# Optimization experiments

Hardware: AMD Instinct MI355X
Metric: run time of the kernel (lower is better)

Reference implementation:

```python
import jax, jax.numpy as jnp
import numpy as np

L = 5  # number of attention+MLP stages

def _layernorm(x, g, b, eps=1e-5):
    mu = x.mean(-1, keepdims=True)
    var = ((x - mu) ** 2).mean(-1, keepdims=True)
    return (x - mu) * jax.lax.rsqrt(var + eps) * g + b

def setup_inputs() -> dict:
    key = jax.random.key(0)
    B, N, C = 8, 2048, 512  # win_size=4, num_slices=12 -> C = 4*4*384//12 = 512
    ks = jax.random.split(key, 7)
    s = 0.02
    return {
        "x": jax.random.normal(ks[0], (B, N, C), dtype=jnp.float32),
        "qkv_w": jax.random.normal(ks[1], (L, C, 3 * C), dtype=jnp.float32) * s,
        "qkv_b": jnp.zeros((L, 3 * C), dtype=jnp.float32),
        "ln_g": jnp.ones((L, C), dtype=jnp.float32),
        "ln_b": jnp.zeros((L, C), dtype=jnp.float32),
        "fc1_w": jax.random.normal(ks[2], (L, C, 2 * C), dtype=jnp.float32) * s,
        "fc1_b": jnp.zeros((L, 2 * C), dtype=jnp.float32),
        "fc2_w": jax.random.normal(ks[3], (L, 2 * C, C), dtype=jnp.float32) * s,
        "fc2_b": jnp.zeros((L, C), dtype=jnp.float32),
    }

def reference(x, qkv_w, qkv_b, ln_g, ln_b, fc1_w, fc1_b, fc2_w, fc2_b):
    B, N, C = x.shape
    half = N // 2
    scale = C ** -0.5  # num_heads = 1 -> head_dim = C
    # Custom block mask: top-left (half x half) block fully visible,
    # top-right block masked; bottom half is tril with diagonal = N//2,
    # i.e. global row i >= half may attend to columns j <= i.
    i = jnp.arange(N)[:, None]
    j = jnp.arange(N)[None, :]
    allowed = jnp.where(i < half, j < half, j <= i)
    bias = jnp.where(allowed, 0.0, -1000.0).astype(x.dtype)  # (N, N)
    for l in range(L):
        # Mask3dAttention (single head)
        qkv = x @ qkv_w[l] + qkv_b[l]                      # (B, N, 3C)
        q, k, v = jnp.split(qkv, 3, axis=-1)               # each (B, N, C)
        attn = jnp.einsum("bnc,bmc->bnm", q * scale, k) + bias
        attn = jax.nn.softmax(attn, axis=-1)
        x = jnp.einsum("bnm,bmc->bnc", attn, v)
        # residual MLP on normed features
        y = _layernorm(x, ln_g[l], ln_b[l])
        h = jax.nn.gelu(y @ fc1_w[l] + fc1_b[l], approximate=False)
        x = x + (h @ fc2_w[l] + fc2_b[l])
    return x
```

## Files before the change

kernel.cpp:

```cpp
#include <hip/hip_runtime.h>
#include <math.h>

typedef unsigned short u16;
typedef __attribute__((ext_vector_type(8))) short bf16x8;
typedef __attribute__((ext_vector_type(4))) float f32x4;
typedef __attribute__((ext_vector_type(4))) unsigned short u16x4;

#define NLAYERS 5
#define BATCH 8
#define SEQ 2048
#define CH 512
#define ROWS_TOTAL (BATCH * SEQ)
#define HALF (SEQ / 2)
#define ATTN_SCALE 0.04419417382415922f

#define SMEM_U16 32768

__device__ __forceinline__ u16 f2bf(float f) {
    unsigned u = __float_as_uint(f);
    u += 0x7fffu + ((u >> 16) & 1u);
    return (u16)(u >> 16);
}

__device__ __forceinline__ u16x4 pack4(f32x4 v) {
    u16x4 o;
    o.x = f2bf(v[0]); o.y = f2bf(v[1]); o.z = f2bf(v[2]); o.w = f2bf(v[3]);
    return o;
}

__device__ __forceinline__ void st16(u16* p, u16x4 v) { *(u16x4*)p = v; }
__device__ __forceinline__ void st16f(float* p, f32x4 v) { *(f32x4*)p = v; }

__device__ __forceinline__ void llds16(const u16* g, u16* l) {
    __builtin_amdgcn_global_load_lds(
        (const __attribute__((address_space(1))) unsigned int*)g,
        (__attribute__((address_space(3))) unsigned int*)l, 16, 0, 0);
}

__device__ __forceinline__ void xcd_rc(int& rt, int& ct) {
    const int n = blockIdx.x;
    const int m = n >> 3;
    rt = (n & 7) * 16 + (m & 15);
    ct = m >> 4;
}

__device__ __forceinline__ void mm_issue(const u16* gA, const u16* gB,
                                         u16* lA, u16* lB, int lda, int ldb)
{
#pragma unroll
    for (int i = 0; i < 4; ++i)
        llds16(gA + (size_t)i * 32 * lda, lA + i * 2048);
#pragma unroll
    for (int i = 0; i < 4; ++i)
        llds16(gB + (size_t)i * 32 * ldb, lB + i * 2048);
}

__device__ __forceinline__ void mm_compute(const u16* As, const u16* Bs,
                                           const int aoff[2][4],
                                           const int boff[2][4],
                                           f32x4 acc[4][4])
{
#pragma unroll
    for (int h = 0; h < 2; ++h) {
        bf16x8 af[4], bfv[4];
#pragma unroll
        for (int t = 0; t < 4; ++t) af[t]  = *(const bf16x8*)&As[aoff[h][t]];
#pragma unroll
        for (int t = 0; t < 4; ++t) bfv[t] = *(const bf16x8*)&Bs[boff[h][t]];
#pragma unroll
        for (int ti = 0; ti < 4; ++ti)
#pragma unroll
            for (int tj = 0; tj < 4; ++tj)
                acc[ti][tj] = __builtin_amdgcn_mfma_f32_16x16x32_bf16(
                    af[ti], bfv[tj], acc[ti][tj], 0, 0, 0);
    }
}

__device__ __forceinline__ void mm_core(
    const u16* __restrict__ A, int lda,
    const u16* __restrict__ Bt, int ldb,
    int row0, int col0, int K,
    u16* SM, f32x4 acc[4][4])
{
    const int tid  = threadIdx.x;
    const int wave = tid >> 6, lane = tid & 63;
    const int wm = (wave & 1) * 64, wn = (wave >> 1) * 64;
    const int q  = lane >> 4,  ln = lane & 15;

    const int sr8 = lane >> 3;
    const int sc  = (lane & 7) ^ sr8;
    const u16* gA = A  + (size_t)(row0 + wave * 8 + sr8) * lda + sc * 8;
    const u16* gB = Bt + (size_t)(col0 + wave * 8 + sr8) * ldb + sc * 8;

    u16* const A0 = SM;
    u16* const B0 = SM + 8192;
    u16* const A1 = SM + 16384;
    u16* const B1 = SM + 24576;
    u16* const w0a = A0 + wave * 512;
    u16* const w0b = B0 + wave * 512;
    u16* const w1a = A1 + wave * 512;
    u16* const w1b = B1 + wave * 512;

    int aoff[2][4], boff[2][4];
#pragma unroll
    for (int h = 0; h < 2; ++h) {
        const int pos = (((h * 4 + q) ^ (ln & 7)) * 8);
#pragma unroll
        for (int t = 0; t < 4; ++t) {
            aoff[h][t] = (wm + t * 16 + ln) * 64 + pos;
            boff[h][t] = (wn + t * 16 + ln) * 64 + pos;
        }
    }

#pragma unroll
    for (int ti = 0; ti < 4; ++ti)
#pragma unroll
        for (int tj = 0; tj < 4; ++tj)
#pragma unroll
            for (int e = 0; e < 4; ++e) acc[ti][tj][e] = 0.f;

    mm_issue(gA, gB, w0a, w0b, lda, ldb);
    gA += 64; gB += 64;

    for (int k0 = 0; k0 < K; k0 += 128) {
        if (k0 + 64 < K) {
            mm_issue(gA, gB, w1a, w1b, lda, ldb);
            gA += 64; gB += 64;
            asm volatile("s_waitcnt vmcnt(8)" ::: "memory");
        } else {
            asm volatile("s_waitcnt vmcnt(0)" ::: "memory");
        }
        __builtin_amdgcn_s_barrier();
        mm_compute(A0, B0, aoff, boff, acc);
        __builtin_amdgcn_s_barrier();
        __builtin_amdgcn_sched_barrier(0);
        if (k0 + 128 < K) {
            mm_issue(gA, gB, w0a, w0b, lda, ldb);
            gA += 64; gB += 64;
            asm volatile("s_waitcnt vmcnt(8)" ::: "memory");
        } else {
            asm volatile("s_waitcnt vmcnt(0)" ::: "memory");
        }
        __builtin_amdgcn_s_barrier();
        mm_compute(A1, B1, aoff, boff, acc);
        __builtin_amdgcn_s_barrier();
        __builtin_amdgcn_sched_barrier(0);
    }
}

template <typename F>
__device__ __forceinline__ void epi_emit(f32x4 acc[4][4], float* eb, F emit)
{
    const int tid = threadIdx.x, wave = tid >> 6, lane = tid & 63;
    const int wn = (wave >> 1) * 64;
    const int q = lane >> 4, ln = lane & 15;
#pragma unroll
    for (int p = 0; p < 4; ++p) {
        __syncthreads();
        if ((wave & 1) == (p >> 1)) {
            const int tibase = (p & 1) * 2;
#pragma unroll
            for (int tj = 0; tj < 4; ++tj)
#pragma unroll
                for (int t2 = 0; t2 < 2; ++t2)
#pragma unroll
                    for (int r = 0; r < 4; ++r)
                        eb[(t2 * 16 + q * 4 + r) * 132 + wn + tj * 16 + ln] =
                            acc[tibase + t2][tj][r];
        }
        __syncthreads();
#pragma unroll
        for (int s = 0; s < 4; ++s) {
            const int row = s * 8 + (tid >> 5);
            const int col = (tid & 31) * 4;
            f32x4 v = *(const f32x4*)&eb[row * 132 + col];
            emit(p * 32 + row, col, v);
        }
    }
}

__global__ __launch_bounds__(256) void qkv_gemm(
    const u16* __restrict__ A, const u16* __restrict__ Bt,
    const float* __restrict__ bias,
    u16* __restrict__ Qb, u16* __restrict__ Kb, u16* __restrict__ Vt)
{
    __shared__ __align__(16) u16 SMEM[SMEM_U16];
    f32x4 acc[4][4];
    int rt, ct; xcd_rc(rt, ct);
    const int row0 = rt * 128, col0 = ct * 128;
    mm_core(A, CH, Bt, CH, row0, col0, CH, SMEM, acc);

    if (ct < 8) {
        u16* dst = (ct < 4) ? Qb : Kb;
        const int cbase = (ct < 4) ? col0 : col0 - CH;
        const float sc = (ct < 4) ? ATTN_SCALE : 1.0f;
        epi_emit(acc, (float*)SMEM, [&](int row, int col, f32x4 v) {
            const float4 bb = *(const float4*)&bias[col0 + col];
            v[0] = (v[0] + bb.x) * sc; v[1] = (v[1] + bb.y) * sc;
            v[2] = (v[2] + bb.z) * sc; v[3] = (v[3] + bb.w) * sc;
            st16(&dst[(size_t)(row0 + row) * CH + cbase + col], pack4(v));
        });
    } else {
        const int tid = threadIdx.x, wave = tid >> 6, lane = tid & 63;
        const int wm = (wave & 1) * 64, wn = (wave >> 1) * 64;
        const int q = lane >> 4, ln = lane & 15;
#pragma unroll
        for (int tj = 0; tj < 4; ++tj) {
            const int gcol = col0 + wn + tj * 16 + ln;
            const float bv = bias[gcol];
#pragma unroll
            for (int ti = 0; ti < 4; ++ti) {
                const int grow = row0 + wm + ti * 16 + q * 4;
                const int b = grow >> 11, j = grow & (SEQ - 1);
                u16x4 o;
                o.x = f2bf(acc[ti][tj][0] + bv);
                o.y = f2bf(acc[ti][tj][1] + bv);
                o.z = f2bf(acc[ti][tj][2] + bv);
                o.w = f2bf(acc[ti][tj][3] + bv);
                st16(&Vt[(size_t)b * CH * SEQ +
                         (size_t)(gcol - 2 * CH) * SEQ + j], o);
            }
        }
    }
}

__global__ __launch_bounds__(256) void qk_gemm(
    const u16* __restrict__ Qb, const u16* __restrict__ Kb,
    u16* __restrict__ Sb, float* __restrict__ rowsum)
{
    const int id = blockIdx.x;
    const int b = id & 7, jt = (id >> 3) & 15, it = id >> 7;
    if (it < 8) { if (jt >= 8) return; } else if (jt > it) return;
    __shared__ __align__(16) u16 SMEM[SMEM_U16];
    f32x4 acc[4][4];
    const u16* A  = Qb + (size_t)b * SEQ * CH;
    const u16* Bt = Kb + (size_t)b * SEQ * CH;
    u16* S = Sb + (size_t)b * SEQ * SEQ;
    const int row0 = it * 128, col0 = jt * 128;
    mm_core(A, CH, Bt, CH, row0, col0, CH, SMEM, acc);

    const bool upper = (it < 8);
    const int tid = threadIdx.x;
    epi_emit(acc, (float*)SMEM, [&](int row, int col, f32x4 v) {
        const int grow = row0 + row;
        const int gcol = col0 + col;
        f32x4 pv;
#pragma unroll
        for (int e = 0; e < 4; ++e) {
            const bool allowed = upper || (gcol + e <= grow);
            pv[e] = allowed ? __expf(fminf(v[e], 60.f)) : 0.f;
        }
        st16(&S[(size_t)grow * SEQ + gcol], pack4(pv));
        float rs = pv[0] + pv[1] + pv[2] + pv[3];
        rs += __shfl_xor(rs, 1, 64);
        rs += __shfl_xor(rs, 2, 64);
        rs += __shfl_xor(rs, 4, 64);
        rs += __shfl_xor(rs, 8, 64);
        rs += __shfl_xor(rs, 16, 64);
        if ((tid & 31) == 0)
            atomicAdd(&rowsum[b * SEQ + grow], rs);
    });
}

__global__ __launch_bounds__(256) void pv_gemm(
    const u16* __restrict__ Sb, const u16* __restrict__ Vt,
    const float* __restrict__ rowsum, float* __restrict__ O)
{
    const int n = blockIdx.x;
    const int b = n & 7, m = n >> 3;
    const int it = 15 - (m >> 2), ct = m & 3;
    const int Kfull = ((it < 8) ? 8 : (it + 1)) * 128;
    __shared__ __align__(16) u16 SMEM[SMEM_U16];
    f32x4 acc[4][4];
    const u16* A  = Sb + (size_t)b * SEQ * SEQ;
    const u16* Bt = Vt + (size_t)b * CH * SEQ;
    const int row0 = it * 128, col0 = ct * 128;
    mm_core(A, SEQ, Bt, SEQ, row0, col0, Kfull, SMEM, acc);

    epi_emit(acc, (float*)SMEM, [&](int row, int col, f32x4 v) {
        const int grow = row0 + row;
        const float rden = 1.0f / rowsum[b * SEQ + grow];
        v[0] *= rden; v[1] *= rden; v[2] *= rden; v[3] *= rden;
        st16f(&O[(size_t)(b * SEQ + grow) * CH + col0 + col], v);
    });
}

__global__ __launch_bounds__(256) void fc1_gemm(
    const u16* __restrict__ A, const u16* __restrict__ Bt,
    const float* __restrict__ bias, u16* __restrict__ H)
{
    __shared__ __align__(16) u16 SMEM[SMEM_U16];
    f32x4 acc[4][4];
    int rt, ct; xcd_rc(rt, ct);
    const int row0 = rt * 128, col0 = ct * 128;
    mm_core(A, CH, Bt, CH, row0, col0, CH, SMEM, acc);
    epi_emit(acc, (float*)SMEM, [&](int row, int col, f32x4 v) {
        const float4 bb = *(const float4*)&bias[col0 + col];
        v[0] += bb.x; v[1] += bb.y; v[2] += bb.z; v[3] += bb.w;
#pragma unroll
        for (int e = 0; e < 4; ++e)
            v[e] = 0.5f * v[e] * (1.f + erff(v[e] * 0.70710678118654752f));
        st16(&H[(size_t)(row0 + row) * (2 * CH) + col0 + col], pack4(v));
    });
}

template <bool WRITE_X>
__global__ __launch_bounds__(256) void fc2_gemm(
    const u16* __restrict__ A, const u16* __restrict__ Bt,
    const float* __restrict__ bias, float* __restrict__ X,
    u16* __restrict__ Xb)
{
    __shared__ __align__(16) u16 SMEM[SMEM_U16];
    f32x4 acc[4][4];
    int rt, ct; xcd_rc(rt, ct);
    const int row0 = rt * 128, col0 = ct * 128;
    mm_core(A, 2 * CH, Bt, 2 * CH, row0, col0, 2 * CH, SMEM, acc);
    epi_emit(acc, (float*)SMEM, [&](int row, int col, f32x4 v) {
        const size_t idx = (size_t)(row0 + row) * CH + col0 + col;
        const float4 bb = *(const float4*)&bias[col0 + col];
        const f32x4 xv = *(const f32x4*)&X[idx];
        v[0] += bb.x + xv[0]; v[1] += bb.y + xv[1];
        v[2] += bb.z + xv[2]; v[3] += bb.w + xv[3];
        if (WRITE_X) st16f(&X[idx], v);
        st16(&Xb[idx], pack4(v));
    });
}

__device__ __forceinline__ float block_sum(float v, volatile float* red, int tid)
{
#pragma unroll
    for (int off = 1; off < 64; off <<= 1) v += __shfl_xor(v, off, 64);
    __syncthreads();
    if ((tid & 63) == 0) red[tid >> 6] = v;
    __syncthreads();
    return red[0] + red[1] + red[2] + red[3];
}

__global__ __launch_bounds__(256) void ln_kernel(
    const float* __restrict__ x, const float* __restrict__ g,
    const float* __restrict__ bta, u16* __restrict__ y)
{
    __shared__ float red[4];
    const int tid = threadIdx.x;
    const size_t base = (size_t)blockIdx.x * CH;
    float x0 = x[base + tid];
    float x1 = x[base + 256 + tid];
    float mu = block_sum(x0 + x1, red, tid) * (1.f / CH);
    float d0 = x0 - mu, d1 = x1 - mu;
    float var = block_sum(d0 * d0 + d1 * d1, red, tid) * (1.f / CH);
    float w = 1.f / sqrtf(var + 1e-5f);
    y[base + tid]       = f2bf(d0 * w * g[tid]       + bta[tid]);
    y[base + 256 + tid] = f2bf(d1 * w * g[256 + tid] + bta[256 + tid]);
}

__global__ __launch_bounds__(256) void f2bf_kernel(
    const float* __restrict__ in, u16* __restrict__ out)
{
    const int i = blockIdx.x * 256 + threadIdx.x;
    float4 v = ((const float4*)in)[i];
    ushort4 o;
    o.x = f2bf(v.x); o.y = f2bf(v.y); o.z = f2bf(v.z); o.w = f2bf(v.w);
    ((ushort4*)out)[i] = o;
}

__global__ __launch_bounds__(256) void wtrans_kernel(
    const float* __restrict__ in, u16* __restrict__ out, int K, int N)
{
    __shared__ float tile[32][33];
    const int l = blockIdx.z;
    in  += (size_t)l * K * N;
    out += (size_t)l * K * N;
    const int n0 = blockIdx.x * 32, k0 = blockIdx.y * 32;
    const int r = threadIdx.x >> 3, c4 = (threadIdx.x & 7) * 4;
    float4 v = *(const float4*)&in[(size_t)(k0 + r) * N + n0 + c4];
    tile[r][c4 + 0] = v.x; tile[r][c4 + 1] = v.y;
    tile[r][c4 + 2] = v.z; tile[r][c4 + 3] = v.w;
    __syncthreads();
    ushort4 o;
    o.x = f2bf(tile[c4 + 0][r]); o.y = f2bf(tile[c4 + 1][r]);
    o.z = f2bf(tile[c4 + 2][r]); o.w = f2bf(tile[c4 + 3][r]);
    *(ushort4*)&out[(size_t)(n0 + r) * K + k0 + c4] = o;
}

extern "C" void kernel_launch(void* const* d_in, const int* in_sizes, int n_in,
                              void* d_out, int out_size, void* d_ws, size_t ws_size,
                              hipStream_t stream)
{
    const float* x_in  = (const float*)d_in[0];
    const float* qkv_w = (const float*)d_in[1];
    const float* qkv_b = (const float*)d_in[2];
    const float* ln_g  = (const float*)d_in[3];
    const float* ln_b  = (const float*)d_in[4];
    const float* fc1_w = (const float*)d_in[5];
    const float* fc1_b = (const float*)d_in[6];
    const float* fc2_w = (const float*)d_in[7];
    const float* fc2_b = (const float*)d_in[8];

    float* xbuf = (float*)d_out;

    char* p = (char*)d_ws;
    u16* qkv_wt = (u16*)p; p += (size_t)NLAYERS * 1536 * 512 * 2;
    u16* fc1_wt = (u16*)p; p += (size_t)NLAYERS * 1024 * 512 * 2;
    u16* fc2_wt = (u16*)p; p += (size_t)NLAYERS * 512 * 1024 * 2;
    u16* xb = (u16*)p; p += (size_t)ROWS_TOTAL * CH * 2;
    u16* Qb = (u16*)p; p += (size_t)ROWS_TOTAL * CH * 2;
    u16* Kb = (u16*)p; p += (size_t)ROWS_TOTAL * CH * 2;
    u16* Vt = (u16*)p; p += (size_t)ROWS_TOTAL * CH * 2;
    float* rowsum = (float*)p; p += (size_t)ROWS_TOTAL * 4;
    u16* Sb = (u16*)p;
    u16* yb = Sb;
    u16* hb = Sb + (size_t)ROWS_TOTAL * CH;

    const dim3 blk(256);

    f2bf_kernel<<<dim3(ROWS_TOTAL * CH / 1024), blk, 0, stream>>>(x_in, xb);
    wtrans_kernel<<<dim3(1536 / 32, 512 / 32, NLAYERS), blk, 0, stream>>>(
        qkv_w, qkv_wt, 512, 1536);
    wtrans_kernel<<<dim3(1024 / 32, 512 / 32, NLAYERS), blk, 0, stream>>>(
        fc1_w, fc1_wt, 512, 1024);
    wtrans_kernel<<<dim3(512 / 32, 1024 / 32, NLAYERS), blk, 0, stream>>>(
        fc2_w, fc2_wt, 1024, 512);

    for (int l = 0; l < NLAYERS; ++l) {
        qkv_gemm<<<dim3(128 * 12), blk, 0, stream>>>(
            xb, qkv_wt + (size_t)l * 1536 * 512, qkv_b + (size_t)l * 1536,
            Qb, Kb, Vt);
        hipMemsetAsync(rowsum, 0, (size_t)ROWS_TOTAL * 4, stream);
        qk_gemm<<<dim3(2048), blk, 0, stream>>>(Qb, Kb, Sb, rowsum);
        pv_gemm<<<dim3(512), blk, 0, stream>>>(Sb, Vt, rowsum, xbuf);
        ln_kernel<<<dim3(ROWS_TOTAL), blk, 0, stream>>>(
            xbuf, ln_g + (size_t)l * CH, ln_b + (size_t)l * CH, yb);
        fc1_gemm<<<dim3(128 * 8), blk, 0, stream>>>(
            yb, fc1_wt + (size_t)l * 1024 * 512, fc1_b + (size_t)l * 1024, hb);
        if (l < NLAYERS - 1)
            fc2_gemm<false><<<dim3(128 * 4), blk, 0, stream>>>(
                hb, fc2_wt + (size_t)l * 512 * 1024, fc2_b + (size_t)l * 512,
                xbuf, xb);
        else
            fc2_gemm<true><<<dim3(128 * 4), blk, 0, stream>>>(
                hb, fc2_wt + (size_t)l * 512 * 1024, fc2_b + (size_t)l * 512,
                xbuf, xb);
    }
}
```

Before: 1.072 ms.

## Use 256x256 tiles with 8-wave pipelined GEMM core for QKV, QK and FC1

Adds a new 512-thread GEMM core that computes a 256x256 output tile per block, with each wave holding a 128x64 accumulator. Global-to-LDS loads for the next k-slab are interleaved between MFMA quarter-steps, and the MFMA phases run at raised priority via setprio. QKV, QK^T and FC1 move to this core with fewer, larger blocks, which raises operand reuse and cuts LDS and global traffic per FLOP. The costs are higher register pressure (128 accumulator floats per thread), 128 KB of shared memory per block, and fewer blocks to balance across CUs, especially FC1 with only 256 blocks.

```diff
diff --git a/kernel.cpp b/kernel.cpp
--- a/kernel.cpp
+++ b/kernel.cpp
@@ -15,6 +15,7 @@
 #define ATTN_SCALE 0.04419417382415922f
 
 #define SMEM_U16 32768
+#define SMEM8_U16 65536
 
 __device__ __forceinline__ u16 f2bf(float f) {
     unsigned u = __float_as_uint(f);
@@ -37,180 +38,214 @@
         (__attribute__((address_space(3))) unsigned int*)l, 16, 0, 0);
 }
 
-__device__ __forceinline__ void xcd_rc(int& rt, int& ct) {
-    const int n = blockIdx.x;
-    const int m = n >> 3;
-    rt = (n & 7) * 16 + (m & 15);
-    ct = m >> 4;
-}
-
-__device__ __forceinline__ void mm_issue(const u16* gA, const u16* gB,
-                                         u16* lA, u16* lB, int lda, int ldb)
-{
-#pragma unroll
-    for (int i = 0; i < 4; ++i)
-        llds16(gA + (size_t)i * 32 * lda, lA + i * 2048);
-#pragma unroll
-    for (int i = 0; i < 4; ++i)
-        llds16(gB + (size_t)i * 32 * ldb, lB + i * 2048);
-}
-
-__device__ __forceinline__ void mm_compute(const u16* As, const u16* Bs,
-                                           const int aoff[2][4],
-                                           const int boff[2][4],
-                                           f32x4 acc[4][4])
-{
-#pragma unroll
-    for (int h = 0; h < 2; ++h) {
-        bf16x8 af[4], bfv[4];
-#pragma unroll
-        for (int t = 0; t < 4; ++t) af[t]  = *(const bf16x8*)&As[aoff[h][t]];
-#pragma unroll
-        for (int t = 0; t < 4; ++t) bfv[t] = *(const bf16x8*)&Bs[boff[h][t]];
-#pragma unroll
-        for (int ti = 0; ti < 4; ++ti)
-#pragma unroll
-            for (int tj = 0; tj < 4; ++tj)
-                acc[ti][tj] = __builtin_amdgcn_mfma_f32_16x16x32_bf16(
-                    af[ti], bfv[tj], acc[ti][tj], 0, 0, 0);
-    }
-}
-
-__device__ __forceinline__ void mm_core(
+#define QMF(MH, NH, BFQ)                                                     \
+    _Pragma("unroll")                                                        \
+    for (int ks = 0; ks < 2; ++ks)                                           \
+        _Pragma("unroll")                                                    \
+        for (int i2 = 0; i2 < 4; ++i2)                                       \
+            _Pragma("unroll")                                                \
+            for (int j2 = 0; j2 < 2; ++j2)                                   \
+                acc[(MH)*4 + i2][(NH)*2 + j2] =                              \
+                    __builtin_amdgcn_mfma_f32_16x16x32_bf16(                 \
+                        af[ks][i2], BFQ[ks][j2],                             \
+                        acc[(MH)*4 + i2][(NH)*2 + j2], 0, 0, 0);
+
+__device__ __forceinline__ void mm8_core(
     const u16* __restrict__ A, int lda,
     const u16* __restrict__ Bt, int ldb,
     int row0, int col0, int K,
-    u16* SM, f32x4 acc[4][4])
-{
-    const int tid  = threadIdx.x;
-    const int wave = tid >> 6, lane = tid & 63;
-    const int wm = (wave & 1) * 64, wn = (wave >> 1) * 64;
-    const int q  = lane >> 4,  ln = lane & 15;
-
+    u16* SM, f32x4 acc[8][4])
+{
+    const int tid = threadIdx.x;
+    const int w = tid >> 6, lane = tid & 63;
+    const int wm128 = (w & 1) * 128, wn64 = (w >> 1) * 64;
+    const int q = lane >> 4, ln = lane & 15;
     const int sr8 = lane >> 3;
     const int sc  = (lane & 7) ^ sr8;
-    const u16* gA = A  + (size_t)(row0 + wave * 8 + sr8) * lda + sc * 8;
-    const u16* gB = Bt + (size_t)(col0 + wave * 8 + sr8) * ldb + sc * 8;
+
+    const u16* gA = A  + (size_t)(row0 + w * 8 + sr8) * lda + sc * 8;
+    const u16* gB = Bt + (size_t)(col0 + w * 8 + sr8) * ldb + sc * 8;
 
     u16* const A0 = SM;
-    u16* const B0 = SM + 8192;
-    u16* const A1 = SM + 16384;
-    u16* const B1 = SM + 24576;
-    u16* const w0a = A0 + wave * 512;
-    u16* const w0b = B0 + wave * 512;
-    u16* const w1a = A1 + wave * 512;
-    u16* const w1b = B1 + wave * 512;
-
-    int aoff[2][4], boff[2][4];
-#pragma unroll
-    for (int h = 0; h < 2; ++h) {
-        const int pos = (((h * 4 + q) ^ (ln & 7)) * 8);
-#pragma unroll
-        for (int t = 0; t < 4; ++t) {
-            aoff[h][t] = (wm + t * 16 + ln) * 64 + pos;
-            boff[h][t] = (wn + t * 16 + ln) * 64 + pos;
-        }
-    }
-
-#pragma unroll
-    for (int ti = 0; ti < 4; ++ti)
-#pragma unroll
-        for (int tj = 0; tj < 4; ++tj)
-#pragma unroll
-            for (int e = 0; e < 4; ++e) acc[ti][tj][e] = 0.f;
-
-    mm_issue(gA, gB, w0a, w0b, lda, ldb);
-    gA += 64; gB += 64;
-
-    for (int k0 = 0; k0 < K; k0 += 128) {
-        if (k0 + 64 < K) {
-            mm_issue(gA, gB, w1a, w1b, lda, ldb);
-            gA += 64; gB += 64;
-            asm volatile("s_waitcnt vmcnt(8)" ::: "memory");
-        } else {
-            asm volatile("s_waitcnt vmcnt(0)" ::: "memory");
-        }
-        __builtin_amdgcn_s_barrier();
-        mm_compute(A0, B0, aoff, boff, acc);
-        __builtin_amdgcn_s_barrier();
-        __builtin_amdgcn_sched_barrier(0);
-        if (k0 + 128 < K) {
-            mm_issue(gA, gB, w0a, w0b, lda, ldb);
-            gA += 64; gB += 64;
-            asm volatile("s_waitcnt vmcnt(8)" ::: "memory");
-        } else {
-            asm volatile("s_waitcnt vmcnt(0)" ::: "memory");
-        }
-        __builtin_amdgcn_s_barrier();
-        mm_compute(A1, B1, aoff, boff, acc);
-        __builtin_amdgcn_s_barrier();
-        __builtin_amdgcn_sched_barrier(0);
+    u16* const B0 = SM + 16384;
+    u16* const A1 = SM + 32768;
+    u16* const B1 = SM + 49152;
+    const int w512 = w * 512;
+
+    int poff[2];
+#pragma unroll
+    for (int ks = 0; ks < 2; ++ks) poff[ks] = (((ks * 4 + q) ^ (ln & 7)) * 8);
+    int arow[2][4], brow[2][2];
+#pragma unroll
+    for (int mh = 0; mh < 2; ++mh)
+#pragma unroll
+        for (int i2 = 0; i2 < 4; ++i2)
+            arow[mh][i2] = (wm128 + mh * 64 + i2 * 16 + ln) * 64;
+#pragma unroll
+    for (int nh = 0; nh < 2; ++nh)
+#pragma unroll
+        for (int j2 = 0; j2 < 2; ++j2)
+            brow[nh][j2] = (wn64 + nh * 32 + j2 * 16 + ln) * 64;
+
+#pragma unroll
+    for (int i = 0; i < 8; ++i)
+#pragma unroll
+        for (int j = 0; j < 4; ++j)
+#pragma unroll
+            for (int e = 0; e < 4; ++e) acc[i][j][e] = 0.f;
+
+    const int T = K >> 6;
+
+#pragma unroll
+    for (int i = 0; i < 4; ++i)
+        llds16(gA + (size_t)i * 64 * lda, A0 + i * 4096 + w512);
+#pragma unroll
+    for (int i = 0; i < 4; ++i)
+        llds16(gB + (size_t)i * 64 * ldb, B0 + i * 4096 + w512);
+    llds16(gA + 64,                        A1 + w512);
+    llds16(gA + 64 + (size_t)64 * lda,     A1 + 4096 + w512);
+    asm volatile("s_waitcnt vmcnt(2)" ::: "memory");
+    __builtin_amdgcn_s_barrier();
+
+    bf16x8 af[2][4], bf0[2][2], bf1[2][2];
+
+    auto TILE = [&](int t, u16* cA, u16* cB, u16* nA, u16* nB) {
+        const size_t kn = (size_t)(t + 1) * 64;
+        const size_t k2 = (size_t)(t + 2) * 64;
+        const bool pn = (t + 1 < T), p2 = (t + 2 < T);
+
+#pragma unroll
+        for (int ks = 0; ks < 2; ++ks)
+#pragma unroll
+            for (int i2 = 0; i2 < 4; ++i2)
+                af[ks][i2] = *(const bf16x8*)&cA[arow[0][i2] + poff[ks]];
+#pragma unroll
+        for (int ks = 0; ks < 2; ++ks)
+#pragma unroll
+            for (int j2 = 0; j2 < 2; ++j2)
+                bf0[ks][j2] = *(const bf16x8*)&cB[brow[0][j2] + poff[ks]];
+        if (pn) {
+            llds16(gA + kn + (size_t)128 * lda, nA + 2 * 4096 + w512);
+            llds16(gA + kn + (size_t)192 * lda, nA + 3 * 4096 + w512);
+            llds16(gB + kn,                     nB + w512);
+        }
+        __builtin_amdgcn_s_barrier();
+        __builtin_amdgcn_s_setprio(1);
+        QMF(0, 0, bf0)
+        __builtin_amdgcn_s_setprio(0);
+        __builtin_amdgcn_s_barrier();
+
+#pragma unroll
+        for (int ks = 0; ks < 2; ++ks)
+#pragma unroll
+            for (int j2 = 0; j2 < 2; ++j2)
+                bf1[ks][j2] = *(const bf16x8*)&cB[brow[1][j2] + poff[ks]];
+        if (pn) {
+            llds16(gB + kn + (size_t)64 * ldb,  nB + 4096 + w512);
+            llds16(gB + kn + (size_t)128 * ldb, nB + 2 * 4096 + w512);
+            llds16(gB + kn + (size_t)192 * ldb, nB + 3 * 4096 + w512);
+        }
+        __builtin_amdgcn_s_barrier();
+        __builtin_amdgcn_s_setprio(1);
+        QMF(0, 1, bf1)
+        __builtin_amdgcn_s_setprio(0);
+        __builtin_amdgcn_s_barrier();
+
+#pragma unroll
+        for (int ks = 0; ks < 2; ++ks)
+#pragma unroll
+            for (int i2 = 0; i2 < 4; ++i2)
+                af[ks][i2] = *(const bf16x8*)&cA[arow[1][i2] + poff[ks]];
+        __builtin_amdgcn_s_barrier();
+        __builtin_amdgcn_s_setprio(1);
+        QMF(1, 1, bf1)
+        __builtin_amdgcn_s_setprio(0);
+        __builtin_amdgcn_s_barrier();
+
+        if (p2) {
+            llds16(gA + k2,                    cA + w512);
+            llds16(gA + k2 + (size_t)64 * lda, cA + 4096 + w512);
+        }
+        __builtin_amdgcn_s_setprio(1);
+        QMF(1, 0, bf0)
+        __builtin_amdgcn_s_setprio(0);
+        if (p2)      asm volatile("s_waitcnt vmcnt(2)" ::: "memory");
+        else if (pn) asm volatile("s_waitcnt vmcnt(0)" ::: "memory");
+        __builtin_amdgcn_s_barrier();
+    };
+
+    for (int t = 0; t < T; t += 2) {
+        TILE(t,     A0, B0, A1, B1);
+        TILE(t + 1, A1, B1, A0, B0);
     }
 }
 
 template <typename F>
-__device__ __forceinline__ void epi_emit(f32x4 acc[4][4], float* eb, F emit)
-{
-    const int tid = threadIdx.x, wave = tid >> 6, lane = tid & 63;
-    const int wn = (wave >> 1) * 64;
+__device__ __forceinline__ void epi_emit8(f32x4 acc[8][4], float* eb, F emit)
+{
+    const int tid = threadIdx.x, w = tid >> 6, lane = tid & 63;
+    const int wn64 = (w >> 1) * 64;
     const int q = lane >> 4, ln = lane & 15;
 #pragma unroll
     for (int p = 0; p < 4; ++p) {
         __syncthreads();
-        if ((wave & 1) == (p >> 1)) {
-            const int tibase = (p & 1) * 2;
+        if ((w & 1) == (p >> 1)) {
+            const int tib = (p & 1) * 4;
 #pragma unroll
             for (int tj = 0; tj < 4; ++tj)
 #pragma unroll
-                for (int t2 = 0; t2 < 2; ++t2)
+                for (int t2 = 0; t2 < 4; ++t2)
 #pragma unroll
                     for (int r = 0; r < 4; ++r)
-                        eb[(t2 * 16 + q * 4 + r) * 132 + wn + tj * 16 + ln] =
-                            acc[tibase + t2][tj][r];
+                        eb[(t2 * 16 + q * 4 + r) * 264 + wn64 + tj * 16 + ln] =
+                            acc[tib + t2][tj][r];
         }
         __syncthreads();
 #pragma unroll
-        for (int s = 0; s < 4; ++s) {
-            const int row = s * 8 + (tid >> 5);
-            const int col = (tid & 31) * 4;
-            f32x4 v = *(const f32x4*)&eb[row * 132 + col];
-            emit(p * 32 + row, col, v);
-        }
-    }
-}
-
-__global__ __launch_bounds__(256) void qkv_gemm(
+        for (int s = 0; s < 8; ++s) {
+            const int row = s * 8 + w;
+            const int col = lane * 4;
+            f32x4 v = *(const f32x4*)&eb[row * 264 + col];
+            emit(p * 64 + row, col, v);
+        }
+    }
+}
+
+__global__ __launch_bounds__(512, 2) void qkv_gemm8(
     const u16* __restrict__ A, const u16* __restrict__ Bt,
     const float* __restrict__ bias,
     u16* __restrict__ Qb, u16* __restrict__ Kb, u16* __restrict__ Vt)
 {
-    __shared__ __align__(16) u16 SMEM[SMEM_U16];
-    f32x4 acc[4][4];
-    int rt, ct; xcd_rc(rt, ct);
-    const int row0 = rt * 128, col0 = ct * 128;
-    mm_core(A, CH, Bt, CH, row0, col0, CH, SMEM, acc);
-
-    if (ct < 8) {
-        u16* dst = (ct < 4) ? Qb : Kb;
-        const int cbase = (ct < 4) ? col0 : col0 - CH;
-        const float sc = (ct < 4) ? ATTN_SCALE : 1.0f;
-        epi_emit(acc, (float*)SMEM, [&](int row, int col, f32x4 v) {
+    __shared__ __align__(16) u16 SMEM[SMEM8_U16];
+    f32x4 acc[8][4];
+    const int id = blockIdx.x;
+    const int m = id >> 3;
+    const int rt = (id & 7) * 8 + (m & 7);
+    const int ct = m >> 3;
+    const int row0 = rt * 256, col0 = ct * 256;
+    mm8_core(A, CH, Bt, CH, row0, col0, CH, SMEM, acc);
+
+    if (ct < 4) {
+        u16* dst = (ct < 2) ? Qb : Kb;
+        const int cbase = (ct < 2) ? col0 : col0 - CH;
+        const float sc = (ct < 2) ? ATTN_SCALE : 1.0f;
+        epi_emit8(acc, (float*)SMEM, [&](int row, int col, f32x4 v) {
             const float4 bb = *(const float4*)&bias[col0 + col];
             v[0] = (v[0] + bb.x) * sc; v[1] = (v[1] + bb.y) * sc;
             v[2] = (v[2] + bb.z) * sc; v[3] = (v[3] + bb.w) * sc;
             st16(&dst[(size_t)(row0 + row) * CH + cbase + col], pack4(v));
         });
     } else {
-        const int tid = threadIdx.x, wave = tid >> 6, lane = tid & 63;
-        const int wm = (wave & 1) * 64, wn = (wave >> 1) * 64;
+        const int tid = threadIdx.x, w = tid >> 6, lane = tid & 63;
+        const int wm128 = (w & 1) * 128, wn64 = (w >> 1) * 64;
         const int q = lane >> 4, ln = lane & 15;
 #pragma unroll
         for (int tj = 0; tj < 4; ++tj) {
-            const int gcol = col0 + wn + tj * 16 + ln;
+            const int gcol = col0 + wn64 + tj * 16 + ln;
             const float bv = bias[gcol];
 #pragma unroll
-            for (int ti = 0; ti < 4; ++ti) {
-                const int grow = row0 + wm + ti * 16 + q * 4;
+            for (int ti = 0; ti < 8; ++ti) {
+                const int grow = row0 + wm128 + ti * 16 + q * 4;
                 const int b = grow >> 11, j = grow & (SEQ - 1);
                 u16x4 o;
                 o.x = f2bf(acc[ti][tj][0] + bv);
@@ -224,24 +259,24 @@
     }
 }
 
-__global__ __launch_bounds__(256) void qk_gemm(
+__global__ __launch_bounds__(512, 2) void qk_gemm8(
     const u16* __restrict__ Qb, const u16* __restrict__ Kb,
     u16* __restrict__ Sb, float* __restrict__ rowsum)
 {
     const int id = blockIdx.x;
-    const int b = id & 7, jt = (id >> 3) & 15, it = id >> 7;
-    if (it < 8) { if (jt >= 8) return; } else if (jt > it) return;
-    __shared__ __align__(16) u16 SMEM[SMEM_U16];
-    f32x4 acc[4][4];
+    const int b = id & 7, jt2 = (id >> 3) & 7, it2 = id >> 6;
+    if (it2 < 4) { if (jt2 >= 4) return; } else if (jt2 > it2) return;
+    __shared__ __align__(16) u16 SMEM[SMEM8_U16];
+    f32x4 acc[8][4];
     const u16* A  = Qb + (size_t)b * SEQ * CH;
     const u16* Bt = Kb + (size_t)b * SEQ * CH;
     u16* S = Sb + (size_t)b * SEQ * SEQ;
-    const int row0 = it * 128, col0 = jt * 128;
-    mm_core(A, CH, Bt, CH, row0, col0, CH, SMEM, acc);
-
-    const bool upper = (it < 8);
-    const int tid = threadIdx.x;
-    epi_emit(acc, (float*)SMEM, [&](int row, int col, f32x4 v) {
+    const int row0 = it2 * 256, col0 = jt2 * 256;
+    mm8_core(A, CH, Bt, CH, row0, col0, CH, SMEM, acc);
+
+    const bool upper = (it2 < 4);
+    const int lane = threadIdx.x & 63;
+    epi_emit8(acc, (float*)SMEM, [&](int row, int col, f32x4 v) {
         const int grow = row0 + row;
         const int gcol = col0 + col;
         f32x4 pv;
@@ -257,9 +292,167 @@
         rs += __shfl_xor(rs, 4, 64);
         rs += __shfl_xor(rs, 8, 64);
         rs += __shfl_xor(rs, 16, 64);
-        if ((tid & 31) == 0)
+        rs += __shfl_xor(rs, 32, 64);
+        if (lane == 0)
             atomicAdd(&rowsum[b * SEQ + grow], rs);
     });
+}
+
+__global__ __launch_bounds__(512, 2) void fc1_gemm8(
+    const u16* __restrict__ A, const u16* __restrict__ Bt,
+    const float* __restrict__ bias, u16* __restrict__ H)
+{
+    __shared__ __align__(16) u16 SMEM[SMEM8_U16];
+    f32x4 acc[8][4];
+    const int id = blockIdx.x;
+    const int m = id >> 3;
+    const int rt = (id & 7) * 8 + (m & 7);
+    const int ct = m >> 3;
+    const int row0 = rt * 256, col0 = ct * 256;
+    mm8_core(A, CH, Bt, CH, row0, col0, CH, SMEM, acc);
+    epi_emit8(acc, (float*)SMEM, [&](int row, int col, f32x4 v) {
+        const float4 bb = *(const float4*)&bias[col0 + col];
+        v[0] += bb.x; v[1] += bb.y; v[2] += bb.z; v[3] += bb.w;
+#pragma unroll
+        for (int e = 0; e < 4; ++e)
+            v[e] = 0.5f * v[e] * (1.f + erff(v[e] * 0.70710678118654752f));
+        st16(&H[(size_t)(row0 + row) * (2 * CH) + col0 + col], pack4(v));
+    });
+}
+
+__device__ __forceinline__ void mm_issue(const u16* gA, const u16* gB,
+                                         u16* lA, u16* lB, int lda, int ldb)
+{
+#pragma unroll
+    for (int i = 0; i < 4; ++i)
+        llds16(gA + (size_t)i * 32 * lda, lA + i * 2048);
+#pragma unroll
+    for (int i = 0; i < 4; ++i)
+        llds16(gB + (size_t)i * 32 * ldb, lB + i * 2048);
+}
+
+__device__ __forceinline__ void mm_compute(const u16* As, const u16* Bs,
+                                           const int aoff[2][4],
+                                           const int boff[2][4],
+                                           f32x4 acc[4][4])
+{
+#pragma unroll
+    for (int h = 0; h < 2; ++h) {
+        bf16x8 af[4], bfv[4];
+#pragma unroll
+        for (int t = 0; t < 4; ++t) af[t]  = *(const bf16x8*)&As[aoff[h][t]];
+#pragma unroll
+        for (int t = 0; t < 4; ++t) bfv[t] = *(const bf16x8*)&Bs[boff[h][t]];
+#pragma unroll
+        for (int ti = 0; ti < 4; ++ti)
+#pragma unroll
+            for (int tj = 0; tj < 4; ++tj)
+                acc[ti][tj] = __builtin_amdgcn_mfma_f32_16x16x32_bf16(
+                    af[ti], bfv[tj], acc[ti][tj], 0, 0, 0);
+    }
+}
+
+__device__ __forceinline__ void mm_core(
+    const u16* __restrict__ A, int lda,
+    const u16* __restrict__ Bt, int ldb,
+    int row0, int col0, int K,
+    u16* SM, f32x4 acc[4][4])
+{
+    const int tid  = threadIdx.x;
+    const int wave = tid >> 6, lane = tid & 63;
+    const int wm = (wave & 1) * 64, wn = (wave >> 1) * 64;
+    const int q  = lane >> 4,  ln = lane & 15;
+
+    const int sr8 = lane >> 3;
+    const int sc  = (lane & 7) ^ sr8;
+    const u16* gA = A  + (size_t)(row0 + wave * 8 + sr8) * lda + sc * 8;
+    const u16* gB = Bt + (size_t)(col0 + wave * 8 + sr8) * ldb + sc * 8;
+
+    u16* const A0 = SM;
+    u16* const B0 = SM + 8192;
+    u16* const A1 = SM + 16384;
+    u16* const B1 = SM + 24576;
+    u16* const w0a = A0 + wave * 512;
+    u16* const w0b = B0 + wave * 512;
+    u16* const w1a = A1 + wave * 512;
+    u16* const w1b = B1 + wave * 512;
+
+    int aoff[2][4], boff[2][4];
+#pragma unroll
+    for (int h = 0; h < 2; ++h) {
+        const int pos = (((h * 4 + q) ^ (ln & 7)) * 8);
+#pragma unroll
+        for (int t = 0; t < 4; ++t) {
+            aoff[h][t] = (wm + t * 16 + ln) * 64 + pos;
+            boff[h][t] = (wn + t * 16 + ln) * 64 + pos;
+        }
+    }
+
+#pragma unroll
+    for (int ti = 0; ti < 4; ++ti)
+#pragma unroll
+        for (int tj = 0; tj < 4; ++tj)
+#pragma unroll
+            for (int e = 0; e < 4; ++e) acc[ti][tj][e] = 0.f;
+
+    mm_issue(gA, gB, w0a, w0b, lda, ldb);
+    gA += 64; gB += 64;
+
+    for (int k0 = 0; k0 < K; k0 += 128) {
+        if (k0 + 64 < K) {
+            mm_issue(gA, gB, w1a, w1b, lda, ldb);
+            gA += 64; gB += 64;
+            asm volatile("s_waitcnt vmcnt(8)" ::: "memory");
+        } else {
+            asm volatile("s_waitcnt vmcnt(0)" ::: "memory");
+        }
+        __builtin_amdgcn_s_barrier();
+        mm_compute(A0, B0, aoff, boff, acc);
+        __builtin_amdgcn_s_barrier();
+        __builtin_amdgcn_sched_barrier(0);
+        if (k0 + 128 < K) {
+            mm_issue(gA, gB, w0a, w0b, lda, ldb);
+            gA += 64; gB += 64;
+            asm volatile("s_waitcnt vmcnt(8)" ::: "memory");
+        } else {
+            asm volatile("s_waitcnt vmcnt(0)" ::: "memory");
+        }
+        __builtin_amdgcn_s_barrier();
+        mm_compute(A1, B1, aoff, boff, acc);
+        __builtin_amdgcn_s_barrier();
+        __builtin_amdgcn_sched_barrier(0);
+    }
+}
+
+template <typename F>
+__device__ __forceinline__ void epi_emit(f32x4 acc[4][4], float* eb, F emit)
+{
+    const int tid = threadIdx.x, wave = tid >> 6, lane = tid & 63;
+    const int wn = (wave >> 1) * 64;
+    const int q = lane >> 4, ln = lane & 15;
+#pragma unroll
+    for (int p = 0; p < 4; ++p) {
+        __syncthreads();
+        if ((wave & 1) == (p >> 1)) {
+            const int tibase = (p & 1) * 2;
+#pragma unroll
+            for (int tj = 0; tj < 4; ++tj)
+#pragma unroll
+                for (int t2 = 0; t2 < 2; ++t2)
+#pragma unroll
+                    for (int r = 0; r < 4; ++r)
+                        eb[(t2 * 16 + q * 4 + r) * 132 + wn + tj * 16 + ln] =
+                            acc[tibase + t2][tj][r];
+        }
+        __syncthreads();
+#pragma unroll
+        for (int s = 0; s < 4; ++s) {
+            const int row = s * 8 + (tid >> 5);
+            const int col = (tid & 31) * 4;
+            f32x4 v = *(const f32x4*)&eb[row * 132 + col];
+            emit(p * 32 + row, col, v);
+        }
+    }
 }
 
 __global__ __launch_bounds__(256) void pv_gemm(
@@ -285,23 +478,11 @@
     });
 }
 
-__global__ __launch_bounds__(256) void fc1_gemm(
-    const u16* __restrict__ A, const u16* __restrict__ Bt,
-    const float* __restrict__ bias, u16* __restrict__ H)
-{
-    __shared__ __align__(16) u16 SMEM[SMEM_U16];
-    f32x4 acc[4][4];
-    int rt, ct; xcd_rc(rt, ct);
-    const int row0 = rt * 128, col0 = ct * 128;
-    mm_core(A, CH, Bt, CH, row0, col0, CH, SMEM, acc);
-    epi_emit(acc, (float*)SMEM, [&](int row, int col, f32x4 v) {
-        const float4 bb = *(const float4*)&bias[col0 + col];
-        v[0] += bb.x; v[1] += bb.y; v[2] += bb.z; v[3] += bb.w;
-#pragma unroll
-        for (int e = 0; e < 4; ++e)
-            v[e] = 0.5f * v[e] * (1.f + erff(v[e] * 0.70710678118654752f));
-        st16(&H[(size_t)(row0 + row) * (2 * CH) + col0 + col], pack4(v));
-    });
+__device__ __forceinline__ void xcd_rc(int& rt, int& ct) {
+    const int n = blockIdx.x;
+    const int m = n >> 3;
+    rt = (n & 7) * 16 + (m & 15);
+    ct = m >> 4;
 }
 
 template <bool WRITE_X>
@@ -412,6 +593,7 @@
     u16* hb = Sb + (size_t)ROWS_TOTAL * CH;
 
     const dim3 blk(256);
+    const dim3 blk8(512);
 
     f2bf_kernel<<<dim3(ROWS_TOTAL * CH / 1024), blk, 0, stream>>>(x_in, xb);
     wtrans_kernel<<<dim3(1536 / 32, 512 / 32, NLAYERS), blk, 0, stream>>>(
@@ -422,22 +604,22 @@
         fc2_w, fc2_wt, 1024, 512);
 
     for (int l = 0; l < NLAYERS; ++l) {
-        qkv_gemm<<<dim3(128 * 12), blk, 0, stream>>>(
+        qkv_gemm8<<<dim3(384), blk8, 0, stream>>>(
             xb, qkv_wt + (size_t)l * 1536 * 512, qkv_b + (size_t)l * 1536,
             Qb, Kb, Vt);
         hipMemsetAsync(rowsum, 0, (size_t)ROWS_TOTAL * 4, stream);
-        qk_gemm<<<dim3(2048), blk, 0, stream>>>(Qb, Kb, Sb, rowsum);
+        qk_gemm8<<<dim3(512), blk8, 0, stream>>>(Qb, Kb, Sb, rowsum);
         pv_gemm<<<dim3(512), blk, 0, stream>>>(Sb, Vt, rowsum, xbuf);
         ln_kernel<<<dim3(ROWS_TOTAL), blk, 0, stream>>>(
             xbuf, ln_g + (size_t)l * CH, ln_b + (size_t)l * CH, yb);
-        fc1_gemm<<<dim3(128 * 8), blk, 0, stream>>>(
+        fc1_gemm8<<<dim3(256), blk8, 0, stream>>>(
             yb, fc1_wt + (size_t)l * 1024 * 512, fc1_b + (size_t)l * 1024, hb);
         if (l < NLAYERS - 1)
-            fc2_gemm<false><<<dim3(128 * 4), blk, 0, stream>>>(
+            fc2_gemm<false><<<dim3(512), blk, 0, stream>>>(
                 hb, fc2_wt + (size_t)l * 512 * 1024, fc2_b + (size_t)l * 512,
                 xbuf, xb);
         else
-            fc2_gemm<true><<<dim3(128 * 4), blk, 0, stream>>>(
+            fc2_gemm<true><<<dim3(512), blk, 0, stream>>>(
                 hb, fc2_wt + (size_t)l * 512 * 1024, fc2_b + (size_t)l * 512,
                 xbuf, xb);
     }
```

Result: slower. 1.143 ms (+6.7%).

## Make QK^T kernel persistent with resident Q tile and double-buffered K

Applied to the files above, without the earlier changes.

Replaces the one-tile-per-block QK^T kernel with a persistent kernel of 256 blocks, each walking a contiguous range of the 164 valid tiles per batch. A block keeps the full 128x512 Q row-panel resident in LDS and reloads it only when the tile row changes. K is streamed in double-buffered 64-wide K slices with explicit waitcnt and barrier pipelining. This cuts redundant Q loads and launches of empty blocks, at the cost of 160KB LDS per block (one block per CU) and fewer blocks to hide latency.

```diff
diff --git a/kernel.cpp b/kernel.cpp
--- a/kernel.cpp
+++ b/kernel.cpp
@@ -15,6 +15,8 @@
 #define ATTN_SCALE 0.04419417382415922f
 
 #define SMEM_U16 32768
+#define QRES_U16 65536
+#define KBUF_U16 8192
 
 __device__ __forceinline__ u16 f2bf(float f) {
     unsigned u = __float_as_uint(f);
@@ -224,42 +226,118 @@
     }
 }
 
-__global__ __launch_bounds__(256) void qk_gemm(
+__global__ __launch_bounds__(256) void qk_res(
     const u16* __restrict__ Qb, const u16* __restrict__ Kb,
     u16* __restrict__ Sb, float* __restrict__ rowsum)
 {
-    const int id = blockIdx.x;
-    const int b = id & 7, jt = (id >> 3) & 15, it = id >> 7;
-    if (it < 8) { if (jt >= 8) return; } else if (jt > it) return;
-    __shared__ __align__(16) u16 SMEM[SMEM_U16];
-    f32x4 acc[4][4];
-    const u16* A  = Qb + (size_t)b * SEQ * CH;
-    const u16* Bt = Kb + (size_t)b * SEQ * CH;
-    u16* S = Sb + (size_t)b * SEQ * SEQ;
-    const int row0 = it * 128, col0 = jt * 128;
-    mm_core(A, CH, Bt, CH, row0, col0, CH, SMEM, acc);
-
-    const bool upper = (it < 8);
+    __shared__ __align__(16) u16 SMEM[QRES_U16 + 2 * KBUF_U16];
+    u16* const Qres = SMEM;
+    u16* const K0   = SMEM + QRES_U16;
+    u16* const K1   = SMEM + QRES_U16 + KBUF_U16;
+    float* const eb = (float*)K0;
+
+    const int bid = blockIdx.x;
+    const int b = bid & 7, wi = bid >> 3;
+    const int u0 = (wi * 164) >> 5, u1 = ((wi + 1) * 164) >> 5;
+
     const int tid = threadIdx.x;
-    epi_emit(acc, (float*)SMEM, [&](int row, int col, f32x4 v) {
-        const int grow = row0 + row;
-        const int gcol = col0 + col;
-        f32x4 pv;
-#pragma unroll
-        for (int e = 0; e < 4; ++e) {
-            const bool allowed = upper || (gcol + e <= grow);
-            pv[e] = allowed ? __expf(fminf(v[e], 60.f)) : 0.f;
-        }
-        st16(&S[(size_t)grow * SEQ + gcol], pack4(pv));
-        float rs = pv[0] + pv[1] + pv[2] + pv[3];
-        rs += __shfl_xor(rs, 1, 64);
-        rs += __shfl_xor(rs, 2, 64);
-        rs += __shfl_xor(rs, 4, 64);
-        rs += __shfl_xor(rs, 8, 64);
-        rs += __shfl_xor(rs, 16, 64);
-        if ((tid & 31) == 0)
-            atomicAdd(&rowsum[b * SEQ + grow], rs);
-    });
+    const int wave = tid >> 6, lane = tid & 63;
+    const int wm = (wave & 1) * 64, wn = (wave >> 1) * 64;
+    const int q = lane >> 4, ln = lane & 15;
+    const int sr8 = lane >> 3;
+    const int sc = (lane & 7) ^ sr8;
+    const int w512 = wave * 512;
+
+    const u16* const Qg = Qb + (size_t)b * SEQ * CH;
+    const u16* const Kg = Kb + (size_t)b * SEQ * CH;
+    u16* const S = Sb + (size_t)b * SEQ * SEQ;
+
+    int aoff[2][4], boff[2][4];
+#pragma unroll
+    for (int h = 0; h < 2; ++h) {
+        const int pos = (((h * 4 + q) ^ (ln & 7)) * 8);
+#pragma unroll
+        for (int t = 0; t < 4; ++t) {
+            aoff[h][t] = (wm + t * 16 + ln) * 64 + pos;
+            boff[h][t] = (wn + t * 16 + ln) * 64 + pos;
+        }
+    }
+
+    int cur_it = -1;
+    for (int u = u0; u < u1; ++u) {
+        int it, jt;
+        if (u < 64) { it = u >> 3; jt = u & 7; }
+        else {
+            int v = u - 64; it = 8; int len = 9;
+            while (v >= len) { v -= len; ++len; ++it; }
+            jt = v;
+        }
+
+        if (it != cur_it) {
+            cur_it = it;
+            const u16* gq = Qg + (size_t)(it * 128 + wave * 8 + sr8) * CH
+                               + sc * 8;
+#pragma unroll
+            for (int kb = 0; kb < 8; ++kb)
+#pragma unroll
+                for (int i = 0; i < 4; ++i)
+                    llds16(gq + (size_t)(i * 32) * CH + kb * 64,
+                           Qres + kb * 8192 + i * 2048 + w512);
+        }
+        const u16* gk = Kg + (size_t)(jt * 128 + wave * 8 + sr8) * CH + sc * 8;
+#pragma unroll
+        for (int i = 0; i < 4; ++i)
+            llds16(gk + (size_t)(i * 32) * CH, K0 + i * 2048 + w512);
+
+        f32x4 acc[4][4];
+#pragma unroll
+        for (int ti = 0; ti < 4; ++ti)
+#pragma unroll
+            for (int tj = 0; tj < 4; ++tj)
+#pragma unroll
+                for (int e = 0; e < 4; ++e) acc[ti][tj][e] = 0.f;
+
+#pragma unroll
+        for (int s = 0; s < 8; ++s) {
+            u16* const nbuf = (s & 1) ? K0 : K1;
+            if (s < 7) {
+#pragma unroll
+                for (int i = 0; i < 4; ++i)
+                    llds16(gk + (size_t)(i * 32) * CH + (s + 1) * 64,
+                           nbuf + i * 2048 + w512);
+                asm volatile("s_waitcnt vmcnt(4)" ::: "memory");
+            } else {
+                asm volatile("s_waitcnt vmcnt(0)" ::: "memory");
+            }
+            __builtin_amdgcn_s_barrier();
+            mm_compute(Qres + s * 8192, (s & 1) ? K1 : K0, aoff, boff, acc);
+            __builtin_amdgcn_s_barrier();
+            __builtin_amdgcn_sched_barrier(0);
+        }
+
+        const bool upper = (it < 8);
+        const int row0 = it * 128, col0 = jt * 128;
+        epi_emit(acc, eb, [&](int row, int col, f32x4 v) {
+            const int grow = row0 + row;
+            const int gcol = col0 + col;
+            f32x4 pv;
+#pragma unroll
+            for (int e = 0; e < 4; ++e) {
+                const bool allowed = upper || (gcol + e <= grow);
+                pv[e] = allowed ? __expf(fminf(v[e], 60.f)) : 0.f;
+            }
+            st16(&S[(size_t)grow * SEQ + gcol], pack4(pv));
+            float rs = pv[0] + pv[1] + pv[2] + pv[3];
+            rs += __shfl_xor(rs, 1, 64);
+            rs += __shfl_xor(rs, 2, 64);
+            rs += __shfl_xor(rs, 4, 64);
+            rs += __shfl_xor(rs, 8, 64);
+            rs += __shfl_xor(rs, 16, 64);
+            if ((tid & 31) == 0)
+                atomicAdd(&rowsum[b * SEQ + grow], rs);
+        });
+        __syncthreads();
+    }
 }
 
 __global__ __launch_bounds__(256) void pv_gemm(
@@ -426,7 +504,7 @@
             xb, qkv_wt + (size_t)l * 1536 * 512, qkv_b + (size_t)l * 1536,
             Qb, Kb, Vt);
         hipMemsetAsync(rowsum, 0, (size_t)ROWS_TOTAL * 4, stream);
-        qk_gemm<<<dim3(2048), blk, 0, stream>>>(Qb, Kb, Sb, rowsum);
+        qk_res<<<dim3(256), blk, 0, stream>>>(Qb, Kb, Sb, rowsum);
         pv_gemm<<<dim3(512), blk, 0, stream>>>(Sb, Vt, rowsum, xbuf);
         ln_kernel<<<dim3(ROWS_TOTAL), blk, 0, stream>>>(
             xbuf, ln_g + (size_t)l * CH, ln_b + (size_t)l * CH, yb);
```

After: 1.185 ms. 1.11x slower.
